# Kernel optimization log

Hardware: AMD Instinct MI355X
Metric: run time of the kernel (lower is better)

Reference implementation:

```python
import jax, jax.numpy as jnp
import numpy as np

VAT = 57      # vat_tokens
ACT = 56      # action_num (KV slice start for cross-attn)
H = 16        # num_heads
NG = 3        # n_groups for num_non_act == 768


def setup_inputs() -> dict:
    key = jax.random.key(0)
    ks = jax.random.split(key, 6)
    B, N, C = 64, 825, 1024
    s = 0.02
    return {
        "x": jax.random.normal(ks[0], (B, N, C), dtype=jnp.float32),
        "W_qkv_non": jax.random.normal(ks[1], (C, 3 * C), dtype=jnp.float32) * s,
        "W_q_act": jax.random.normal(ks[2], (C, C), dtype=jnp.float32) * s,
        "W_kv_act": jax.random.normal(ks[3], (C, 2 * C), dtype=jnp.float32) * s,
        "W_proj_non": jax.random.normal(ks[4], (C, C), dtype=jnp.float32) * s,
        "b_proj_non": jnp.zeros((C,), dtype=jnp.float32),
        "W_proj_act": jax.random.normal(ks[5], (C, C), dtype=jnp.float32) * s,
        "b_proj_act": jnp.zeros((C,), dtype=jnp.float32),
    }


def reference(x, W_qkv_non, W_q_act, W_kv_act, W_proj_non, b_proj_non,
              W_proj_act, b_proj_act):
    B, N, C = x.shape
    d = C // H
    scale = d ** -0.5
    nna = N - VAT              # num non-act tokens (768)
    gs = nna // NG             # group size (256)

    # --- grouped windowed self-attention over non-act tokens ---
    non = x[:, VAT:].reshape(B, NG, gs, C)
    qkv = (non @ W_qkv_non).reshape(B, NG, gs, 3, H, d)
    q, k, v = jnp.moveaxis(qkv, 3, 0)           # each [B, NG, gs, H, d]
    q = q.transpose(0, 1, 3, 2, 4)              # [B, NG, H, gs, d]
    k = k.transpose(0, 1, 3, 2, 4)
    v = v.transpose(0, 1, 3, 2, 4)
    attn = jax.nn.softmax(jnp.einsum('bghqd,bghkd->bghqk', q, k) * scale, axis=-1)
    x_non = jnp.einsum('bghqk,bghkd->bghqd', attn, v)
    x_non = x_non.transpose(0, 1, 3, 2, 4).reshape(B, nna, C)

    # --- cross-attention: act queries attend to KV subset [ACT:] of all tokens ---
    q_act = (x[:, :VAT] @ W_q_act).reshape(B, VAT, H, d).transpose(0, 2, 1, 3)
    kv = (x @ W_kv_act).reshape(B, N, 2, H, d)
    k_act = kv[:, ACT:, 0].transpose(0, 2, 1, 3)   # [B, H, N-ACT, d]
    v_act = kv[:, ACT:, 1].transpose(0, 2, 1, 3)
    attn_a = jax.nn.softmax(jnp.einsum('bhqd,bhkd->bhqk', q_act, k_act) * scale, axis=-1)
    x_act = jnp.einsum('bhqk,bhkd->bhqd', attn_a, v_act)
    x_act = x_act.transpose(0, 2, 1, 3).reshape(B, VAT, C)

    # --- output projections + concat [act, non] ---
    x_non = x_non @ W_proj_non + b_proj_non
    x_act = x_act @ W_proj_act + b_proj_act
    return jnp.concatenate([x_act, x_non], axis=1)
```

## Files before the change

kernel.cpp:

```cpp
#include <hip/hip_runtime.h>
#include <stdint.h>


typedef __attribute__((ext_vector_type(8))) unsigned short u16x8;
typedef __attribute__((ext_vector_type(8))) _Float16 f16x8;
typedef __attribute__((ext_vector_type(4))) float f32x4;

__device__ __forceinline__ unsigned short f2h(float f) {
  _Float16 h = (_Float16)f;
  return __builtin_bit_cast(unsigned short, h);
}

__device__ __forceinline__ float exp2r(float x) {
  return __builtin_amdgcn_exp2f(x);
}

__device__ __forceinline__ void mfma16(f32x4& d, u16x8 a, u16x8 b) {
  d = __builtin_amdgcn_mfma_f32_16x16x32_f16(
      __builtin_bit_cast(f16x8, a), __builtin_bit_cast(f16x8, b), d, 0, 0, 0);
}

__device__ __forceinline__ void async16(void* lds_p, const void* g) {
  __builtin_amdgcn_global_load_lds(
      (const __attribute__((address_space(1))) unsigned int*)g,
      (__attribute__((address_space(3))) unsigned int*)lds_p, 16, 0, 0);
}

__device__ __forceinline__ int swz(int row, int bcol) {
  return (row << 7) + (bcol ^ ((row & 7) << 4));
}

__device__ __forceinline__ int xcd_swz(int bid, int nwg) {
  int q8 = nwg >> 3, r8 = nwg & 7;
  int xcd = bid & 7, idx = bid >> 3;
  return (xcd < r8 ? xcd * (q8 + 1) : r8 * (q8 + 1) + (xcd - r8) * q8) + idx;
}

static constexpr size_t OFF_XB   = 0;
static constexpr size_t OFF_QKV  = 108134400;
static constexpr size_t OFF_KV   = 410124288;
static constexpr size_t OFF_QACT = 611713024;
static constexpr size_t OFF_ANON = 619184128;
static constexpr size_t OFF_AACT = 719847424;
static constexpr size_t OFF_WQKV = 727318528;
static constexpr size_t OFF_WKV  = 733609984;
static constexpr size_t OFF_WQ   = 737804288;
static constexpr size_t OFF_WPN  = 739901440;
static constexpr size_t OFF_WPA  = 741998592;

__global__ __launch_bounds__(256) void k_cast(const float* __restrict__ in,
                                              unsigned short* __restrict__ outp,
                                              int n8) {
  int stride = gridDim.x * 256;
  for (int i = blockIdx.x * 256 + threadIdx.x; i < n8; i += stride) {
    float4 v0 = ((const float4*)in)[i * 2];
    float4 v1 = ((const float4*)in)[i * 2 + 1];
    uint4 w;
    w.x = (unsigned)f2h(v0.x) | ((unsigned)f2h(v0.y) << 16);
    w.y = (unsigned)f2h(v0.z) | ((unsigned)f2h(v0.w) << 16);
    w.z = (unsigned)f2h(v1.x) | ((unsigned)f2h(v1.y) << 16);
    w.w = (unsigned)f2h(v1.z) | ((unsigned)f2h(v1.w) << 16);
    ((uint4*)outp)[i] = w;
  }
}

__global__ __launch_bounds__(256) void k_tc5(
    const float* __restrict__ Wqkv, const float* __restrict__ Wkv,
    const float* __restrict__ Wq,   const float* __restrict__ Wpn,
    const float* __restrict__ Wpa,
    unsigned short* __restrict__ Tqkv, unsigned short* __restrict__ Tkv,
    unsigned short* __restrict__ Tq,   unsigned short* __restrict__ Tpn,
    unsigned short* __restrict__ Tpa) {
  __shared__ float ts[32][33];
  int bx = blockIdx.x;
  const float* W; unsigned short* Wt; int Nc, nb;
  if (bx < 96)       { W = Wqkv; Wt = Tqkv; Nc = 3072; nb = bx; }
  else if (bx < 160) { W = Wkv;  Wt = Tkv;  Nc = 2048; nb = bx - 96; }
  else if (bx < 192) { W = Wq;   Wt = Tq;   Nc = 1024; nb = bx - 160; }
  else if (bx < 224) { W = Wpn;  Wt = Tpn;  Nc = 1024; nb = bx - 192; }
  else               { W = Wpa;  Wt = Tpa;  Nc = 1024; nb = bx - 224; }
  int n0 = nb * 32, k0 = blockIdx.y * 32;
  int tx = threadIdx.x & 31, ty = threadIdx.x >> 5;
#pragma unroll
  for (int i = 0; i < 4; i++) {
    int k = ty + i * 8;
    ts[k][tx] = W[(size_t)(k0 + k) * Nc + n0 + tx];
  }
  __syncthreads();
#pragma unroll
  for (int i = 0; i < 4; i++) {
    int n = ty + i * 8;
    Wt[(size_t)(n0 + n) * 1024 + k0 + tx] = f2h(ts[tx][n]);
  }
}

template <int EPI>
__device__ __forceinline__ void gemm256_body(
    const unsigned short* __restrict__ A, const unsigned short* __restrict__ Bt,
    const float* __restrict__ bias, void* __restrict__ outp,
    int M, int NTN, int arpb, int aoff, int ldo, int orpb, int ooff,
    int wg, char* lds) {
  int tid = threadIdx.x, lane = tid & 63, wid = tid >> 6;
  int fr = lane & 15, fg = lane >> 4;

  int mt = wg / NTN, nt = wg - mt * NTN;
  int r0 = mt << 8, n0 = nt << 8;
  if (r0 > M - 256) r0 = M - 256;

  const unsigned short* pA[2][2];
  const unsigned short* pB[2][2];
#pragma unroll
  for (int j = 0; j < 2; j++) {
    int rc = (wid * 2 + j) * 8 + (lane >> 3);
    int cc = (lane & 7) ^ (rc & 7);
#pragma unroll
    for (int a = 0; a < 2; a++) {
      int row = (rc >> 6) * 128 + a * 64 + (rc & 63);
      int r = r0 + row;
      if (r >= M) r = M - 1;
      size_t gr;
      if (arpb > 0) { int bb = r / arpb; gr = (size_t)bb * 825 + aoff + (r - bb * arpb); }
      else gr = (size_t)r;
      pA[a][j] = A + gr * 1024 + cc * 8;
    }
#pragma unroll
    for (int b = 0; b < 2; b++) {
      int n = ((rc >> 5) & 3) * 64 + b * 32 + (rc & 31);
      pB[b][j] = Bt + (size_t)(n0 + n) * 1024 + cc * 8;
    }
  }

  int wr = wid >> 2, wc = wid & 3;
  int ch0 = fg ^ (fr & 7);
  int aoff0 = (wr * 64 + fr) * 128 + ch0 * 16;
  int boff0 = (wc * 32 + fr) * 128 + ch0 * 16;

  u16x8 afr[8], bf0[4], bf1[4];
  f32x4 acc[8][4] = {};

#define BAR  asm volatile("s_barrier" ::: "memory")
#define VM6  asm volatile("s_waitcnt vmcnt(6)" ::: "memory")
#define VM0  asm volatile("s_waitcnt vmcnt(0)" ::: "memory")

  auto LDA = [&](int d, int a) {
    char* base = lds + d * 65536 + a * 16384;
#pragma unroll
    for (int mm = 0; mm < 4; mm++)
#pragma unroll
      for (int ks = 0; ks < 2; ks++)
        afr[mm * 2 + ks] = *(const u16x8*)(base + mm * 2048 + (aoff0 ^ (ks * 64)));
  };
  auto LDB = [&](int d, int b, u16x8* bf) {
    char* base = lds + d * 65536 + 32768 + b * 16384;
#pragma unroll
    for (int nn = 0; nn < 2; nn++)
#pragma unroll
      for (int ks = 0; ks < 2; ks++)
        bf[nn * 2 + ks] = *(const u16x8*)(base + nn * 2048 + (boff0 ^ (ks * 64)));
  };
  auto STAGE_A = [&](int d, int a, int t) {
#pragma unroll
    for (int j = 0; j < 2; j++)
      async16(lds + d * 65536 + a * 16384 + ((wid * 2 + j) << 10), pA[a][j] + t * 64);
  };
  auto STAGE_B = [&](int d, int b, int t) {
#pragma unroll
    for (int j = 0; j < 2; j++)
      async16(lds + d * 65536 + 32768 + b * 16384 + ((wid * 2 + j) << 10), pB[b][j] + t * 64);
  };
  auto CLUSTER = [&](int a, int b, u16x8* bf) {
    __builtin_amdgcn_s_setprio(1);
#pragma unroll
    for (int mm = 0; mm < 4; mm++)
#pragma unroll
      for (int nn = 0; nn < 2; nn++)
#pragma unroll
        for (int ks = 0; ks < 2; ks++)
          mfma16(acc[a * 4 + mm][b * 2 + nn], afr[mm * 2 + ks], bf[nn * 2 + ks]);
    __builtin_amdgcn_s_setprio(0);
  };

  STAGE_A(0, 0, 0); STAGE_B(0, 0, 0); STAGE_B(0, 1, 0); STAGE_A(0, 1, 0);
  STAGE_A(1, 0, 1); STAGE_B(1, 0, 1); STAGE_B(1, 1, 1);
  VM6; BAR;

#pragma unroll 1
  for (int i = 0; i < 8; i++) {
    bool nl = (i < 7);
    int t1 = 2 * i + 1, t2 = 2 * i + 2, t3 = 2 * i + 3;
    LDA(0, 0); LDB(0, 0, bf0);
    STAGE_A(1, 1, t1);
    CLUSTER(0, 0, bf0); BAR;
    LDB(0, 1, bf1);
    if (nl) STAGE_A(0, 0, t2);
    CLUSTER(0, 1, bf1);
    LDA(0, 1);
    if (nl) STAGE_B(0, 0, t2);
    CLUSTER(1, 0, bf0); BAR;
    if (nl) STAGE_B(0, 1, t2);
    CLUSTER(1, 1, bf1);
    if (nl) { VM6; } else { VM0; }
    BAR;
    LDA(1, 0); LDB(1, 0, bf0);
    if (nl) STAGE_A(0, 1, t2);
    CLUSTER(0, 0, bf0); BAR;
    LDB(1, 1, bf1);
    if (nl) STAGE_A(1, 0, t3);
    CLUSTER(0, 1, bf1);
    LDA(1, 1);
    if (nl) STAGE_B(1, 0, t3);
    CLUSTER(1, 0, bf0); BAR;
    if (nl) STAGE_B(1, 1, t3);
    CLUSTER(1, 1, bf1);
    if (nl) { VM6; } else { VM0; }
    BAR;
  }
#undef BAR
#undef VM6
#undef VM0

  int coln[4];
#pragma unroll
  for (int n = 0; n < 4; n++)
    coln[n] = n0 + wc * 64 + (n >> 1) * 32 + (n & 1) * 16 + fr;
  if (EPI == 0) {
    unsigned short* o = (unsigned short*)outp;
#pragma unroll
    for (int m = 0; m < 8; m++)
#pragma unroll
      for (int reg = 0; reg < 4; reg++) {
        int r = r0 + wr * 128 + (m >> 2) * 64 + (m & 3) * 16 + (lane >> 4) * 4 + reg;
        if (r < M) {
          size_t base = (size_t)r * ldo;
#pragma unroll
          for (int n = 0; n < 4; n++) o[base + coln[n]] = f2h(acc[m][n][reg]);
        }
      }
  } else {
    float* o = (float*)outp;
#pragma unroll
    for (int m = 0; m < 8; m++)
#pragma unroll
      for (int reg = 0; reg < 4; reg++) {
        int r = r0 + wr * 128 + (m >> 2) * 64 + (m & 3) * 16 + (lane >> 4) * 4 + reg;
        if (r < M) {
          int bb = r / orpb;
          size_t orow = (size_t)bb * 825 + ooff + (r - bb * orpb);
          size_t base = orow * 1024;
#pragma unroll
          for (int n = 0; n < 4; n++)
            o[base + coln[n]] = acc[m][n][reg] + bias[coln[n]];
        }
      }
  }
}

__global__ __launch_bounds__(512, 2) void k_gemm_in(
    const unsigned short* __restrict__ xb,
    const unsigned short* __restrict__ WtQKV,
    const unsigned short* __restrict__ WtKV,
    const unsigned short* __restrict__ WtQ,
    unsigned short* __restrict__ qkv, unsigned short* __restrict__ kvb,
    unsigned short* __restrict__ qact) {
  extern __shared__ char lds[];
  int bid = blockIdx.x;
  if (bid < 2304) {
    gemm256_body<0>(xb, WtQKV, nullptr, qkv, 49152, 12, 768, 57, 3072, 0, 0,
                    xcd_swz(bid, 2304), lds);
  } else if (bid < 3848) {
    gemm256_body<0>(xb, WtKV, nullptr, kvb, 49216, 8, 769, 56, 2048, 0, 0,
                    xcd_swz(bid - 2304, 1544), lds);
  } else {
    gemm256_body<0>(xb, WtQ, nullptr, qact, 3648, 4, 57, 0, 1024, 0, 0,
                    xcd_swz(bid - 3848, 60), lds);
  }
}

template <int EPI>
__global__ __launch_bounds__(512, 2) void k_gemm256(
    const unsigned short* __restrict__ A, const unsigned short* __restrict__ Bt,
    const float* __restrict__ bias, void* __restrict__ outp,
    int M, int NTN, int arpb, int aoff, int ldo, int orpb, int ooff) {
  extern __shared__ char lds[];
  gemm256_body<EPI>(A, Bt, bias, outp, M, NTN, arpb, aoff, ldo, orpb, ooff,
                    xcd_swz(blockIdx.x, gridDim.x), lds);
}

template <int EPI>
__global__ __launch_bounds__(256, 2) void k_gemm(
    const unsigned short* __restrict__ A, const unsigned short* __restrict__ Bt,
    const float* __restrict__ bias, void* __restrict__ outp,
    int M, int Nn, int arpb, int aoff, int ldo, int orpb, int ooff) {
  __shared__ __align__(16) unsigned short As[128 * 32];
  __shared__ __align__(16) unsigned short Bs[128 * 32];
  int tid = threadIdx.x, lane = tid & 63, wid = tid >> 6;
  int NT = Nn >> 7;
  int mt = blockIdx.x / NT, nt = blockIdx.x - mt * NT;
  int r0 = mt << 7, n0 = nt << 7;

  const unsigned short* aptr[2];
  const unsigned short* bptr[2];
#pragma unroll
  for (int i = 0; i < 2; i++) {
    int c = tid + (i << 8);
    int r = r0 + (c >> 2);
    if (r >= M) r = M - 1;
    size_t gr;
    if (arpb > 0) { int bb = r / arpb; gr = (size_t)bb * 825 + aoff + (r - bb * arpb); }
    else gr = (size_t)r;
    aptr[i] = A + gr * 1024 + (c & 3) * 8;
    bptr[i] = Bt + (size_t)(n0 + (c >> 2)) * 1024 + (c & 3) * 8;
  }
  char* AsB = (char*)As;
  char* BsB = (char*)Bs;
  int wr = wid >> 1, wc = wid & 1;
  int fr = lane & 15, fcol = (lane >> 4) * 16;
  f32x4 acc[4][4] = {};

  for (int kk = 0; kk < 1024; kk += 32) {
    async16(AsB + (wid << 10), aptr[0] + kk);
    async16(AsB + 4096 + (wid << 10), aptr[1] + kk);
    async16(BsB + (wid << 10), bptr[0] + kk);
    async16(BsB + 4096 + (wid << 10), bptr[1] + kk);
    __syncthreads();
    u16x8 af[4], bfv[4];
#pragma unroll
    for (int m = 0; m < 4; m++)
      af[m] = *(const u16x8*)(AsB + (wr * 64 + m * 16 + fr) * 64 + fcol);
#pragma unroll
    for (int n = 0; n < 4; n++)
      bfv[n] = *(const u16x8*)(BsB + (wc * 64 + n * 16 + fr) * 64 + fcol);
#pragma unroll
    for (int m = 0; m < 4; m++)
#pragma unroll
      for (int n = 0; n < 4; n++) mfma16(acc[m][n], af[m], bfv[n]);
    __syncthreads();
  }

  int cb = wc * 64 + fr;
  int rb = wr * 64 + (lane >> 4) * 4;
  if (EPI == 0) {
    unsigned short* o = (unsigned short*)outp;
#pragma unroll
    for (int m = 0; m < 4; m++)
#pragma unroll
      for (int reg = 0; reg < 4; reg++) {
        int r = r0 + rb + m * 16 + reg;
        if (r < M) {
          size_t base = (size_t)r * ldo + n0 + cb;
#pragma unroll
          for (int n = 0; n < 4; n++) o[base + n * 16] = f2h(acc[m][n][reg]);
        }
      }
  } else {
    float* o = (float*)outp;
#pragma unroll
    for (int m = 0; m < 4; m++)
#pragma unroll
      for (int reg = 0; reg < 4; reg++) {
        int r = r0 + rb + m * 16 + reg;
        if (r < M) {
          int bb = r / orpb;
          size_t orow = (size_t)bb * 825 + ooff + (r - bb * orpb);
          size_t base = orow * 1024 + n0 + cb;
#pragma unroll
          for (int n = 0; n < 4; n++)
            o[base + n * 16] = acc[m][n][reg] + bias[n0 + cb + n * 16];
        }
      }
  }
}

static constexpr float C1 = 0.125f * 1.44269504089f;

__device__ __forceinline__ void attn_non_body(
    const unsigned short* __restrict__ qkv, unsigned short* __restrict__ aout,
    int bid, char* smem) {
  int h = bid & 15, t = bid >> 4;
  int g = t % 3, b = t / 3;
  int tid = threadIdx.x, lane = tid & 63, wid = tid >> 6;
  int fr = lane & 15, fg = lane >> 4;
  size_t rowbase = (size_t)(b * 768 + g * 256);
  const unsigned short* Qb = qkv + rowbase * 3072 + h * 64;
  const unsigned short* Kb = Qb + 1024;
  const unsigned short* Vb = Qb + 2048;

  char* Vt0 = smem;
  char* Pw = smem + 16384 + wid * 8192;

  int qr = wid * 64;
  u16x8 qf[4][2];
#pragma unroll
  for (int mq = 0; mq < 4; mq++)
#pragma unroll
    for (int ks = 0; ks < 2; ks++)
      qf[mq][ks] = *(const u16x8*)(Qb + (size_t)(qr + mq * 16 + fr) * 3072 + ks * 32 + fg * 8);

  f32x4 o[4][4] = {};
  float mrun[4], lrun[4];
#pragma unroll
  for (int mq = 0; mq < 4; mq++) { mrun[mq] = -1e30f; lrun[mq] = 0.f; }

  int vpr = lane & 31;
  int vcc = wid * 2 + (lane >> 5);
  const unsigned short* Vp = Vb + (size_t)(2 * vpr) * 3072 + vcc * 8;

  u16x8 v0 = *(const u16x8*)(Vp);
  u16x8 v1 = *(const u16x8*)(Vp + 3072);
  u16x8 kf[2][4];
#pragma unroll
  for (int kt = 0; kt < 4; kt++)
#pragma unroll
    for (int ks = 0; ks < 2; ks++)
      kf[ks][kt] = *(const u16x8*)(Kb + (size_t)(kt * 16 + fr) * 3072 + ks * 32 + fg * 8);

  {
#pragma unroll
    for (int j = 0; j < 8; j++) {
      unsigned pk = (unsigned)v0[j] | ((unsigned)v1[j] << 16);
      *(unsigned*)(Vt0 + swz(vcc * 8 + j, 4 * vpr)) = pk;
    }
    v0 = *(const u16x8*)(Vp + (size_t)64 * 3072);
    v1 = *(const u16x8*)(Vp + (size_t)65 * 3072);
  }

  for (int c = 0; c < 4; c++) {
    __syncthreads();
    if (c < 3) {
      char* VtN = Vt0 + ((c + 1) & 1) * 8192;
#pragma unroll
      for (int j = 0; j < 8; j++) {
        unsigned pk = (unsigned)v0[j] | ((unsigned)v1[j] << 16);
        *(unsigned*)(VtN + swz(vcc * 8 + j, 4 * vpr)) = pk;
      }
      if (c < 2) {
        v0 = *(const u16x8*)(Vp + (size_t)(c + 2) * 64 * 3072);
        v1 = *(const u16x8*)(Vp + (size_t)((c + 2) * 64 + 1) * 3072);
      }
    }

    f32x4 s[4][4] = {};
#pragma unroll
    for (int ks = 0; ks < 2; ks++)
#pragma unroll
      for (int kt = 0; kt < 4; kt++)
#pragma unroll
        for (int mq = 0; mq < 4; mq++) mfma16(s[kt][mq], kf[ks][kt], qf[mq][ks]);
    if (c < 3) {
#pragma unroll
      for (int kt = 0; kt < 4; kt++)
#pragma unroll
        for (int ks = 0; ks < 2; ks++)
          kf[ks][kt] = *(const u16x8*)(Kb + (size_t)((c + 1) * 64 + kt * 16 + fr) * 3072 + ks * 32 + fg * 8);
    }

#pragma unroll
    for (int mq = 0; mq < 4; mq++) {
      float v = -1e30f;
#pragma unroll
      for (int kt = 0; kt < 4; kt++)
#pragma unroll
        for (int reg = 0; reg < 4; reg++) v = fmaxf(v, s[kt][mq][reg]);
      v = fmaxf(v, __shfl_xor(v, 16));
      v = fmaxf(v, __shfl_xor(v, 32));
      v *= C1;
      if (!__all(v <= mrun[mq] + 8.f)) {
        float mn = fmaxf(mrun[mq], v);
        float alpha = exp2r(mrun[mq] - mn);
        mrun[mq] = mn;
        lrun[mq] *= alpha;
#pragma unroll
        for (int dt = 0; dt < 4; dt++) o[dt][mq] *= alpha;
      }
      float mn = mrun[mq];
      int q = mq * 16 + fr;
      float rs = 0.f;
#pragma unroll
      for (int kt = 0; kt < 4; kt++) {
        f32x4 p;
#pragma unroll
        for (int reg = 0; reg < 4; reg++)
          p[reg] = exp2r(fmaf(s[kt][mq][reg], C1, -mn));
        rs += p[0] + p[1] + p[2] + p[3];
        uint2 w;
        w.x = (unsigned)f2h(p[0]) | ((unsigned)f2h(p[1]) << 16);
        w.y = (unsigned)f2h(p[2]) | ((unsigned)f2h(p[3]) << 16);
        *(uint2*)(Pw + swz(q, kt * 32 + fg * 8)) = w;
      }
      rs += __shfl_xor(rs, 16);
      rs += __shfl_xor(rs, 32);
      lrun[mq] += rs;
    }
    char* VtB = Vt0 + (c & 1) * 8192;
#pragma unroll
    for (int ks = 0; ks < 2; ks++) {
      u16x8 vf[4], pf[4];
#pragma unroll
      for (int dt = 0; dt < 4; dt++)
        vf[dt] = *(const u16x8*)(VtB + swz(dt * 16 + fr, ks * 64 + fg * 16));
#pragma unroll
      for (int mq = 0; mq < 4; mq++)
        pf[mq] = *(const u16x8*)(Pw + swz(mq * 16 + fr, ks * 64 + fg * 16));
#pragma unroll
      for (int dt = 0; dt < 4; dt++)
#pragma unroll
        for (int mq = 0; mq < 4; mq++) mfma16(o[dt][mq], vf[dt], pf[mq]);
    }
  }

#pragma unroll
  for (int mq = 0; mq < 4; mq++) {
    float rl = 1.0f / lrun[mq];
    size_t row = rowbase + qr + mq * 16 + fr;
#pragma unroll
    for (int dt = 0; dt < 4; dt++) {
      uint2 w;
      w.x = (unsigned)f2h(o[dt][mq][0] * rl) | ((unsigned)f2h(o[dt][mq][1] * rl) << 16);
      w.y = (unsigned)f2h(o[dt][mq][2] * rl) | ((unsigned)f2h(o[dt][mq][3] * rl) << 16);
      *(uint2*)(aout + row * 1024 + h * 64 + dt * 16 + fg * 4) = w;
    }
  }
}

__device__ __forceinline__ void attn_act_body(
    const unsigned short* __restrict__ qa, const unsigned short* __restrict__ kv,
    unsigned short* __restrict__ aout, int bid, char* smem) {
  int h = bid & 15, b = bid >> 4;
  int tid = threadIdx.x, lane = tid & 63, wid = tid >> 6;
  int fr = lane & 15, fg = lane >> 4;
  const unsigned short* Qb = qa + (size_t)b * 57 * 1024 + h * 64;
  const unsigned short* Kb = kv + (size_t)b * 769 * 2048 + h * 64;
  const unsigned short* Vb = Kb + 1024;

  char* Vw = smem + wid * 8192;
  char* Pw = smem + 32768 + wid * 8192;
  float* Ml = (float*)(smem + 65536);
  float* Ll = (float*)(smem + 65536 + 1024);

  u16x8 qf[4][2];
#pragma unroll
  for (int mq = 0; mq < 4; mq++) {
    int q = mq * 16 + fr;
    if (q > 56) q = 56;
#pragma unroll
    for (int ks = 0; ks < 2; ks++)
      qf[mq][ks] = *(const u16x8*)(Qb + (size_t)q * 1024 + ks * 32 + fg * 8);
  }
  f32x4 o[4][4] = {};
  float mrun[4], lrun[4];
#pragma unroll
  for (int mq = 0; mq < 4; mq++) { mrun[mq] = -1e30f; lrun[mq] = 0.f; }

  u16x8 kf[2][4];
  {
    int kc0 = wid * 64;
#pragma unroll
    for (int kt = 0; kt < 4; kt++) {
      int krow = kc0 + kt * 16 + fr;
      if (krow > 768) krow = 768;
#pragma unroll
      for (int ks = 0; ks < 2; ks++)
        kf[ks][kt] = *(const u16x8*)(Kb + (size_t)krow * 2048 + ks * 32 + fg * 8);
    }
  }

  int vpr = lane & 31;
  for (int c = wid; c < 13; c += 4) {
    int kc0 = c * 64;
#pragma unroll
    for (int i = 0; i < 4; i++) {
      int cv = i * 2 + (lane >> 5);
      int kr0 = kc0 + 2 * vpr, kr1 = kc0 + 2 * vpr + 1;
      if (kr0 > 768) kr0 = 768;
      if (kr1 > 768) kr1 = 768;
      u16x8 v0 = *(const u16x8*)(Vb + (size_t)kr0 * 2048 + cv * 8);
      u16x8 v1 = *(const u16x8*)(Vb + (size_t)kr1 * 2048 + cv * 8);
#pragma unroll
      for (int j = 0; j < 8; j++) {
        unsigned pk = (unsigned)v0[j] | ((unsigned)v1[j] << 16);
        *(unsigned*)(Vw + swz(cv * 8 + j, 4 * vpr)) = pk;
      }
    }

    f32x4 s[4][4] = {};
#pragma unroll
    for (int ks = 0; ks < 2; ks++)
#pragma unroll
      for (int kt = 0; kt < 4; kt++)
#pragma unroll
        for (int mq = 0; mq < 4; mq++) mfma16(s[kt][mq], kf[ks][kt], qf[mq][ks]);
    if (c + 4 < 13) {
      int kn = (c + 4) * 64;
#pragma unroll
      for (int kt = 0; kt < 4; kt++) {
        int krow = kn + kt * 16 + fr;
        if (krow > 768) krow = 768;
#pragma unroll
        for (int ks = 0; ks < 2; ks++)
          kf[ks][kt] = *(const u16x8*)(Kb + (size_t)krow * 2048 + ks * 32 + fg * 8);
      }
    }
    if (kc0 + 64 > 769) {
#pragma unroll
      for (int kt = 0; kt < 4; kt++)
#pragma unroll
        for (int reg = 0; reg < 4; reg++)
          if (kc0 + kt * 16 + fg * 4 + reg >= 769)
#pragma unroll
            for (int mq = 0; mq < 4; mq++) s[kt][mq][reg] = -1e30f;
    }

#pragma unroll
    for (int mq = 0; mq < 4; mq++) {
      float v = -1e30f;
#pragma unroll
      for (int kt = 0; kt < 4; kt++)
#pragma unroll
        for (int reg = 0; reg < 4; reg++) v = fmaxf(v, s[kt][mq][reg]);
      v = fmaxf(v, __shfl_xor(v, 16));
      v = fmaxf(v, __shfl_xor(v, 32));
      v *= C1;
      if (!__all(v <= mrun[mq] + 8.f)) {
        float mn = fmaxf(mrun[mq], v);
        float alpha = exp2r(mrun[mq] - mn);
        mrun[mq] = mn;
        lrun[mq] *= alpha;
#pragma unroll
        for (int dt = 0; dt < 4; dt++) o[dt][mq] *= alpha;
      }
      float mn = mrun[mq];
      int q = mq * 16 + fr;
      float rs = 0.f;
#pragma unroll
      for (int kt = 0; kt < 4; kt++) {
        f32x4 p;
#pragma unroll
        for (int reg = 0; reg < 4; reg++)
          p[reg] = exp2r(fmaf(s[kt][mq][reg], C1, -mn));
        rs += p[0] + p[1] + p[2] + p[3];
        uint2 w;
        w.x = (unsigned)f2h(p[0]) | ((unsigned)f2h(p[1]) << 16);
        w.y = (unsigned)f2h(p[2]) | ((unsigned)f2h(p[3]) << 16);
        *(uint2*)(Pw + swz(q, kt * 32 + fg * 8)) = w;
      }
      rs += __shfl_xor(rs, 16);
      rs += __shfl_xor(rs, 32);
      lrun[mq] += rs;
    }
#pragma unroll
    for (int ks = 0; ks < 2; ks++) {
      u16x8 vf[4], pf[4];
#pragma unroll
      for (int dt = 0; dt < 4; dt++)
        vf[dt] = *(const u16x8*)(Vw + swz(dt * 16 + fr, ks * 64 + fg * 16));
#pragma unroll
      for (int mq = 0; mq < 4; mq++)
        pf[mq] = *(const u16x8*)(Pw + swz(mq * 16 + fr, ks * 64 + fg * 16));
#pragma unroll
      for (int dt = 0; dt < 4; dt++)
#pragma unroll
        for (int mq = 0; mq < 4; mq++) mfma16(o[dt][mq], vf[dt], pf[mq]);
    }
  }

  __syncthreads();
  if (fg == 0) {
#pragma unroll
    for (int mq = 0; mq < 4; mq++) {
      Ml[wid * 64 + mq * 16 + fr] = mrun[mq];
      Ll[wid * 64 + mq * 16 + fr] = lrun[mq];
    }
  }
  __syncthreads();
  float* Oac = (float*)smem;
  for (int i = tid; i < 4096; i += 256) Oac[i] = 0.f;
  __syncthreads();
  for (int w = 0; w < 4; w++) {
    if (wid == w) {
#pragma unroll
      for (int mq = 0; mq < 4; mq++) {
        int q = mq * 16 + fr;
        float Mq = fmaxf(fmaxf(Ml[q], Ml[64 + q]), fmaxf(Ml[128 + q], Ml[192 + q]));
        float f = exp2r(mrun[mq] - Mq);
#pragma unroll
        for (int dt = 0; dt < 4; dt++) {
          int d = dt * 16 + fg * 4;
#pragma unroll
          for (int reg = 0; reg < 4; reg++)
            Oac[(d + reg) * 64 + q] += o[dt][mq][reg] * f;
        }
      }
    }
    __syncthreads();
  }
  for (int i = tid; i < 4096; i += 256) {
    int d = i >> 6, q = i & 63;
    if (q < 57) {
      float Mq = fmaxf(fmaxf(Ml[q], Ml[64 + q]), fmaxf(Ml[128 + q], Ml[192 + q]));
      float Lq = Ll[q] * exp2r(Ml[q] - Mq) + Ll[64 + q] * exp2r(Ml[64 + q] - Mq) +
                 Ll[128 + q] * exp2r(Ml[128 + q] - Mq) + Ll[192 + q] * exp2r(Ml[192 + q] - Mq);
      aout[(size_t)(b * 57 + q) * 1024 + h * 64 + d] = f2h(Oac[i] / Lq);
    }
  }
}

__global__ __launch_bounds__(256, 2) void k_attn(
    const unsigned short* __restrict__ qkv, const unsigned short* __restrict__ qa,
    const unsigned short* __restrict__ kv,
    unsigned short* __restrict__ anon, unsigned short* __restrict__ aact) {
  extern __shared__ char smem[];
  int bid = blockIdx.x;
  if (bid < 1024) attn_act_body(qa, kv, aact, bid, smem);
  else            attn_non_body(qkv, anon, bid - 1024, smem);
}

extern "C" void kernel_launch(void* const* d_in, const int* in_sizes, int n_in,
                              void* d_out, int out_size, void* d_ws, size_t ws_size,
                              hipStream_t stream) {
  const float* x    = (const float*)d_in[0];
  const float* Wqkv = (const float*)d_in[1];
  const float* Wq   = (const float*)d_in[2];
  const float* Wkv  = (const float*)d_in[3];
  const float* Wpn  = (const float*)d_in[4];
  const float* bpn  = (const float*)d_in[5];
  const float* Wpa  = (const float*)d_in[6];
  const float* bpa  = (const float*)d_in[7];
  float* out = (float*)d_out;
  char* ws = (char*)d_ws;

  unsigned short* xb   = (unsigned short*)(ws + OFF_XB);
  unsigned short* qkv  = (unsigned short*)(ws + OFF_QKV);
  unsigned short* kvb  = (unsigned short*)(ws + OFF_KV);
  unsigned short* qact = (unsigned short*)(ws + OFF_QACT);
  unsigned short* anon = (unsigned short*)(ws + OFF_ANON);
  unsigned short* aact = (unsigned short*)(ws + OFF_AACT);
  unsigned short* WtQKV = (unsigned short*)(ws + OFF_WQKV);
  unsigned short* WtKV  = (unsigned short*)(ws + OFF_WKV);
  unsigned short* WtQ   = (unsigned short*)(ws + OFF_WQ);
  unsigned short* WtPN  = (unsigned short*)(ws + OFF_WPN);
  unsigned short* WtPA  = (unsigned short*)(ws + OFF_WPA);

  hipFuncSetAttribute((const void*)k_gemm_in,
                      hipFuncAttributeMaxDynamicSharedMemorySize, 131072);
  hipFuncSetAttribute((const void*)k_gemm256<1>,
                      hipFuncAttributeMaxDynamicSharedMemorySize, 131072);
  hipFuncSetAttribute((const void*)k_attn,
                      hipFuncAttributeMaxDynamicSharedMemorySize, 67584);

  k_cast<<<2048, 256, 0, stream>>>(x, xb, 6758400);
  k_tc5<<<dim3(256, 32), 256, 0, stream>>>(Wqkv, Wkv, Wq, Wpn, Wpa,
                                           WtQKV, WtKV, WtQ, WtPN, WtPA);

  k_gemm_in<<<3908, 512, 131072, stream>>>(xb, WtQKV, WtKV, WtQ,
                                           qkv, kvb, qact);

  k_attn<<<4096, 256, 67584, stream>>>(qkv, qact, kvb, anon, aact);

  k_gemm256<1><<<192 * 4, 512, 131072, stream>>>(anon, WtPN, bpn, out,
                                                 49152, 4, 0, 0, 1024, 768, 57);
  k_gemm<1><<<29 * 8, 256, 0, stream>>>(aact, WtPA, bpa, out,
                                        3648, 1024, 0, 0, 1024, 57, 0);
}
```

Before: 945.1 us.

## Halve GEMM K-tile to 32 with half LDS, and merge cast and transpose kernels

The 256x256 GEMM body now stages K-steps of 32 halves instead of 64. That halves LDS use to 64KB per block, which may allow two blocks per CU, and it changes the swizzle, the fragment counts and the wait counts to match. The trade is twice as many pipeline iterations, more barriers per unit of work and fewer MFMAs between syncs. Separately, the x cast and the weight transpose kernels are merged into one launch to save a kernel launch.

Measured after the change: 1.000 ms. +5.9%, slower.

```diff
diff --git a/kernel.cpp b/kernel.cpp
--- a/kernel.cpp
+++ b/kernel.cpp
@@ -48,38 +48,39 @@
 static constexpr size_t OFF_WPN  = 739901440;
 static constexpr size_t OFF_WPA  = 741998592;
 
-__global__ __launch_bounds__(256) void k_cast(const float* __restrict__ in,
-                                              unsigned short* __restrict__ outp,
-                                              int n8) {
-  int stride = gridDim.x * 256;
-  for (int i = blockIdx.x * 256 + threadIdx.x; i < n8; i += stride) {
-    float4 v0 = ((const float4*)in)[i * 2];
-    float4 v1 = ((const float4*)in)[i * 2 + 1];
-    uint4 w;
-    w.x = (unsigned)f2h(v0.x) | ((unsigned)f2h(v0.y) << 16);
-    w.y = (unsigned)f2h(v0.z) | ((unsigned)f2h(v0.w) << 16);
-    w.z = (unsigned)f2h(v1.x) | ((unsigned)f2h(v1.y) << 16);
-    w.w = (unsigned)f2h(v1.z) | ((unsigned)f2h(v1.w) << 16);
-    ((uint4*)outp)[i] = w;
-  }
-}
-
-__global__ __launch_bounds__(256) void k_tc5(
+__global__ __launch_bounds__(256) void k_prep(
+    const float* __restrict__ x, unsigned short* __restrict__ xb, int n8,
     const float* __restrict__ Wqkv, const float* __restrict__ Wkv,
     const float* __restrict__ Wq,   const float* __restrict__ Wpn,
     const float* __restrict__ Wpa,
     unsigned short* __restrict__ Tqkv, unsigned short* __restrict__ Tkv,
     unsigned short* __restrict__ Tq,   unsigned short* __restrict__ Tpn,
     unsigned short* __restrict__ Tpa) {
+  int bxg = blockIdx.x;
+  if (bxg < 2048) {
+    int stride = 2048 * 256;
+    for (int i = bxg * 256 + threadIdx.x; i < n8; i += stride) {
+      float4 v0 = ((const float4*)x)[i * 2];
+      float4 v1 = ((const float4*)x)[i * 2 + 1];
+      uint4 w;
+      w.x = (unsigned)f2h(v0.x) | ((unsigned)f2h(v0.y) << 16);
+      w.y = (unsigned)f2h(v0.z) | ((unsigned)f2h(v0.w) << 16);
+      w.z = (unsigned)f2h(v1.x) | ((unsigned)f2h(v1.y) << 16);
+      w.w = (unsigned)f2h(v1.z) | ((unsigned)f2h(v1.w) << 16);
+      ((uint4*)xb)[i] = w;
+    }
+    return;
+  }
   __shared__ float ts[32][33];
-  int bx = blockIdx.x;
+  int bx2 = bxg - 2048;
+  int bx = bx2 & 255, ky = bx2 >> 8;
   const float* W; unsigned short* Wt; int Nc, nb;
   if (bx < 96)       { W = Wqkv; Wt = Tqkv; Nc = 3072; nb = bx; }
   else if (bx < 160) { W = Wkv;  Wt = Tkv;  Nc = 2048; nb = bx - 96; }
   else if (bx < 192) { W = Wq;   Wt = Tq;   Nc = 1024; nb = bx - 160; }
   else if (bx < 224) { W = Wpn;  Wt = Tpn;  Nc = 1024; nb = bx - 192; }
   else               { W = Wpa;  Wt = Tpa;  Nc = 1024; nb = bx - 224; }
-  int n0 = nb * 32, k0 = blockIdx.y * 32;
+  int n0 = nb * 32, k0 = ky * 32;
   int tx = threadIdx.x & 31, ty = threadIdx.x >> 5;
 #pragma unroll
   for (int i = 0; i < 4; i++) {
@@ -107,66 +108,55 @@
   int r0 = mt << 8, n0 = nt << 8;
   if (r0 > M - 256) r0 = M - 256;
 
-  const unsigned short* pA[2][2];
-  const unsigned short* pB[2][2];
-#pragma unroll
-  for (int j = 0; j < 2; j++) {
-    int rc = (wid * 2 + j) * 8 + (lane >> 3);
-    int cc = (lane & 7) ^ (rc & 7);
-#pragma unroll
-    for (int a = 0; a < 2; a++) {
-      int row = (rc >> 6) * 128 + a * 64 + (rc & 63);
-      int r = r0 + row;
-      if (r >= M) r = M - 1;
-      size_t gr;
-      if (arpb > 0) { int bb = r / arpb; gr = (size_t)bb * 825 + aoff + (r - bb * arpb); }
-      else gr = (size_t)r;
-      pA[a][j] = A + gr * 1024 + cc * 8;
-    }
-#pragma unroll
-    for (int b = 0; b < 2; b++) {
-      int n = ((rc >> 5) & 3) * 64 + b * 32 + (rc & 31);
-      pB[b][j] = Bt + (size_t)(n0 + n) * 1024 + cc * 8;
-    }
+  int rc = tid >> 2;
+  int cc = (tid & 3) ^ ((rc >> 1) & 3);
+  const unsigned short* pA[2];
+  const unsigned short* pB[2];
+#pragma unroll
+  for (int a = 0; a < 2; a++) {
+    int row = (rc >> 6) * 128 + a * 64 + (rc & 63);
+    int r = r0 + row;
+    if (r >= M) r = M - 1;
+    size_t gr;
+    if (arpb > 0) { int bb = r / arpb; gr = (size_t)bb * 825 + aoff + (r - bb * arpb); }
+    else gr = (size_t)r;
+    pA[a] = A + gr * 1024 + cc * 8;
+  }
+#pragma unroll
+  for (int b = 0; b < 2; b++) {
+    int n = ((rc >> 5) & 3) * 64 + b * 32 + (rc & 31);
+    pB[b] = Bt + (size_t)(n0 + n) * 1024 + cc * 8;
   }
 
   int wr = wid >> 2, wc = wid & 3;
-  int ch0 = fg ^ (fr & 7);
-  int aoff0 = (wr * 64 + fr) * 128 + ch0 * 16;
-  int boff0 = (wc * 32 + fr) * 128 + ch0 * 16;
-
-  u16x8 afr[8], bf0[4], bf1[4];
+  int ch0 = fg ^ ((fr >> 1) & 3);
+  int aoff0 = (wr * 64 + fr) * 64 + ch0 * 16;
+  int boff0 = (wc * 32 + fr) * 64 + ch0 * 16;
+
+  u16x8 afr[4], bf0[2], bf1[2];
   f32x4 acc[8][4] = {};
 
 #define BAR  asm volatile("s_barrier" ::: "memory")
-#define VM6  asm volatile("s_waitcnt vmcnt(6)" ::: "memory")
+#define VM3  asm volatile("s_waitcnt vmcnt(3)" ::: "memory")
 #define VM0  asm volatile("s_waitcnt vmcnt(0)" ::: "memory")
 
   auto LDA = [&](int d, int a) {
-    char* base = lds + d * 65536 + a * 16384;
+    char* base = lds + d * 32768 + a * 8192;
 #pragma unroll
     for (int mm = 0; mm < 4; mm++)
-#pragma unroll
-      for (int ks = 0; ks < 2; ks++)
-        afr[mm * 2 + ks] = *(const u16x8*)(base + mm * 2048 + (aoff0 ^ (ks * 64)));
+      afr[mm] = *(const u16x8*)(base + mm * 1024 + aoff0);
   };
   auto LDB = [&](int d, int b, u16x8* bf) {
-    char* base = lds + d * 65536 + 32768 + b * 16384;
+    char* base = lds + d * 32768 + 16384 + b * 8192;
 #pragma unroll
     for (int nn = 0; nn < 2; nn++)
-#pragma unroll
-      for (int ks = 0; ks < 2; ks++)
-        bf[nn * 2 + ks] = *(const u16x8*)(base + nn * 2048 + (boff0 ^ (ks * 64)));
+      bf[nn] = *(const u16x8*)(base + nn * 1024 + boff0);
   };
   auto STAGE_A = [&](int d, int a, int t) {
-#pragma unroll
-    for (int j = 0; j < 2; j++)
-      async16(lds + d * 65536 + a * 16384 + ((wid * 2 + j) << 10), pA[a][j] + t * 64);
+    async16(lds + d * 32768 + a * 8192 + (wid << 10), pA[a] + t * 32);
   };
   auto STAGE_B = [&](int d, int b, int t) {
-#pragma unroll
-    for (int j = 0; j < 2; j++)
-      async16(lds + d * 65536 + 32768 + b * 16384 + ((wid * 2 + j) << 10), pB[b][j] + t * 64);
+    async16(lds + d * 32768 + 16384 + b * 8192 + (wid << 10), pB[b] + t * 32);
   };
   auto CLUSTER = [&](int a, int b, u16x8* bf) {
     __builtin_amdgcn_s_setprio(1);
@@ -174,19 +164,17 @@
     for (int mm = 0; mm < 4; mm++)
 #pragma unroll
       for (int nn = 0; nn < 2; nn++)
-#pragma unroll
-        for (int ks = 0; ks < 2; ks++)
-          mfma16(acc[a * 4 + mm][b * 2 + nn], afr[mm * 2 + ks], bf[nn * 2 + ks]);
+        mfma16(acc[a * 4 + mm][b * 2 + nn], afr[mm], bf[nn]);
     __builtin_amdgcn_s_setprio(0);
   };
 
   STAGE_A(0, 0, 0); STAGE_B(0, 0, 0); STAGE_B(0, 1, 0); STAGE_A(0, 1, 0);
   STAGE_A(1, 0, 1); STAGE_B(1, 0, 1); STAGE_B(1, 1, 1);
-  VM6; BAR;
+  VM3; BAR;
 
 #pragma unroll 1
-  for (int i = 0; i < 8; i++) {
-    bool nl = (i < 7);
+  for (int i = 0; i < 16; i++) {
+    bool nl = (i < 15);
     int t1 = 2 * i + 1, t2 = 2 * i + 2, t3 = 2 * i + 3;
     LDA(0, 0); LDB(0, 0, bf0);
     STAGE_A(1, 1, t1);
@@ -199,7 +187,7 @@
     CLUSTER(1, 0, bf0); BAR;
     if (nl) STAGE_B(0, 1, t2);
     CLUSTER(1, 1, bf1);
-    if (nl) { VM6; } else { VM0; }
+    if (nl) { VM3; } else { VM0; }
     BAR;
     LDA(1, 0); LDB(1, 0, bf0);
     if (nl) STAGE_A(0, 1, t2);
@@ -212,11 +200,11 @@
     CLUSTER(1, 0, bf0); BAR;
     if (nl) STAGE_B(1, 1, t3);
     CLUSTER(1, 1, bf1);
-    if (nl) { VM6; } else { VM0; }
+    if (nl) { VM3; } else { VM0; }
     BAR;
   }
 #undef BAR
-#undef VM6
+#undef VM3
 #undef VM0
 
   int coln[4];
@@ -741,23 +729,22 @@
   unsigned short* WtPA  = (unsigned short*)(ws + OFF_WPA);
 
   hipFuncSetAttribute((const void*)k_gemm_in,
-                      hipFuncAttributeMaxDynamicSharedMemorySize, 131072);
+                      hipFuncAttributeMaxDynamicSharedMemorySize, 65536);
   hipFuncSetAttribute((const void*)k_gemm256<1>,
-                      hipFuncAttributeMaxDynamicSharedMemorySize, 131072);
+                      hipFuncAttributeMaxDynamicSharedMemorySize, 65536);
   hipFuncSetAttribute((const void*)k_attn,
                       hipFuncAttributeMaxDynamicSharedMemorySize, 67584);
 
-  k_cast<<<2048, 256, 0, stream>>>(x, xb, 6758400);
-  k_tc5<<<dim3(256, 32), 256, 0, stream>>>(Wqkv, Wkv, Wq, Wpn, Wpa,
-                                           WtQKV, WtKV, WtQ, WtPN, WtPA);
-
-  k_gemm_in<<<3908, 512, 131072, stream>>>(xb, WtQKV, WtKV, WtQ,
-                                           qkv, kvb, qact);
+  k_prep<<<10240, 256, 0, stream>>>(x, xb, 6758400, Wqkv, Wkv, Wq, Wpn, Wpa,
+                                    WtQKV, WtKV, WtQ, WtPN, WtPA);
+
+  k_gemm_in<<<3908, 512, 65536, stream>>>(xb, WtQKV, WtKV, WtQ,
+                                          qkv, kvb, qact);
 
   k_attn<<<4096, 256, 67584, stream>>>(qkv, qact, kvb, anon, aact);
 
-  k_gemm256<1><<<192 * 4, 512, 131072, stream>>>(anon, WtPN, bpn, out,
-                                                 49152, 4, 0, 0, 1024, 768, 57);
+  k_gemm256<1><<<192 * 4, 512, 65536, stream>>>(anon, WtPN, bpn, out,
+                                                49152, 4, 0, 0, 1024, 768, 57);
   k_gemm<1><<<29 * 8, 256, 0, stream>>>(aact, WtPA, bpa, out,
                                         3648, 1024, 0, 0, 1024, 57, 0);
 }
```
